# Kernel optimization log

Hardware: AMD Instinct MI355X
Metric: run time of the kernel (lower is better)

## Reference

```python
import jax, jax.numpy as jnp
import numpy as np

N, E, H, IN = 4096, 65536, 256, 16
N_BLOCKS, N_SUB = 3, 2
IE = 2 * H + 2  # edge-mlp input: h[row] ++ h[col] ++ edge_attr(2)
NORM_FACTOR = 100.0


def setup_inputs() -> dict:
    key = jax.random.key(0)
    ks = jax.random.split(key, 24)
    G = N_BLOCKS * N_SUB  # 6 GCLs total

    def p(k, shape, fan_in, gain=1.0):
        return gain * jax.random.normal(k, shape, jnp.float32) / np.sqrt(fan_in)

    return {
        "h": jax.random.normal(ks[0], (N, IN), jnp.float32),
        "x": jax.random.normal(ks[1], (N, 3), jnp.float32),
        "edge_index": jax.random.randint(ks[2], (2, E), 0, N),
        # embedding in/out
        "emb_w": p(ks[3], (IN, H), IN), "emb_b": jnp.zeros((H,), jnp.float32),
        "out_w": p(ks[4], (H, IN), H), "out_b": jnp.zeros((IN,), jnp.float32),
        # GCL edge MLP (stacked over the 6 GCLs)
        "edge_w1": p(ks[5], (G, IE, H), IE), "edge_b1": jnp.zeros((G, H), jnp.float32),
        "edge_w2": p(ks[6], (G, H, H), H), "edge_b2": jnp.zeros((G, H), jnp.float32),
        # GCL node MLP
        "node_w1": p(ks[7], (G, 2 * H, H), 2 * H), "node_b1": jnp.zeros((G, H), jnp.float32),
        "node_w2": p(ks[8], (G, H, H), H), "node_b2": jnp.zeros((G, H), jnp.float32),
        # EquivariantUpdate coord MLP (stacked over 3 blocks); last layer xavier gain=0.001, no bias
        "coord_w1": p(ks[9], (N_BLOCKS, IE, H), IE), "coord_b1": jnp.zeros((N_BLOCKS, H), jnp.float32),
        "coord_w2": p(ks[10], (N_BLOCKS, H, H), H), "coord_b2": jnp.zeros((N_BLOCKS, H), jnp.float32),
        "coord_w3": p(ks[11], (N_BLOCKS, H, 1), H, gain=0.001),
    }


def reference(h, x, edge_index, emb_w, emb_b, out_w, out_b,
              edge_w1, edge_b1, edge_w2, edge_b2,
              node_w1, node_b1, node_w2, node_b2,
              coord_w1, coord_b1, coord_w2, coord_b2, coord_w3):
    row, col = edge_index[0], edge_index[1]
    n_nodes = h.shape[0]

    def seg_sum(data):  # unsorted_segment_sum with 'sum' aggregation / normalization_factor
        return jax.ops.segment_sum(data, row, num_segments=n_nodes) / NORM_FACTOR

    def coord2diff(xc):  # norm_constant = 1
        d = xc[row] - xc[col]                      # [E,3]
        radial = jnp.sum(d * d, axis=1, keepdims=True)  # [E,1]
        cd = d / (jnp.sqrt(radial + 1e-8) + 1.0)
        return radial, cd

    dist0, _ = coord2diff(x)          # EGNN-level distances (from initial coords)
    h = h @ emb_w + emb_b             # node embedding

    gi = 0
    for b in range(N_BLOCKS):
        radial, coord_diff = coord2diff(x)
        ea = jnp.concatenate([radial, dist0], axis=1)   # [E,2] edge_attr
        for _ in range(N_SUB):  # GCL sublayers
            m = jnp.concatenate([h[row], h[col], ea], axis=1)           # [E, 2H+2]
            m = jax.nn.silu(m @ edge_w1[gi] + edge_b1[gi])
            m = jax.nn.silu(m @ edge_w2[gi] + edge_b2[gi])              # [E, H]
            agg = seg_sum(m)                                            # [N, H]
            u = jnp.concatenate([h, agg], axis=1)                       # [N, 2H]
            u = jax.nn.silu(u @ node_w1[gi] + node_b1[gi])
            h = h + u @ node_w2[gi] + node_b2[gi]                       # residual node update
            gi += 1
        # EquivariantUpdate (tanh=False)
        t = jnp.concatenate([h[row], h[col], ea], axis=1)
        t = jax.nn.silu(t @ coord_w1[b] + coord_b1[b])
        t = jax.nn.silu(t @ coord_w2[b] + coord_b2[b])
        trans = coord_diff * (t @ coord_w3[b])                          # [E,3]
        x = x + seg_sum(trans)

    h = h @ out_w + out_b
    return h, x
```

## Files before the change

kernel.cpp:

```cpp
#include <hip/hip_runtime.h>
#include <hip/hip_bf16.h>
#include <cstdint>
#include <cstddef>

#define NN 4096
#define NE 65536
#define HD 256

typedef __attribute__((ext_vector_type(4))) float f32x4;
typedef __attribute__((ext_vector_type(8))) __bf16 bf16x8;

static __device__ __forceinline__ float silu_f(float v) {
  return v / (1.f + __expf(-v));
}

struct TJob { const float* src; __bf16* dst; int K; int N; };
struct TJobs { TJob j[39]; };

__global__ __launch_bounds__(256) void k_transpose(TJobs jobs) {
  TJob jb = jobs.j[blockIdx.z];
  int k0 = blockIdx.x << 5, n0 = blockIdx.y << 5;
  if (k0 >= jb.K || n0 >= jb.N) return;
  __shared__ float t[32][33];
  int tx = threadIdx.x & 31, ty = threadIdx.x >> 5;
#pragma unroll
  for (int r = ty; r < 32; r += 8)
    t[r][tx] = jb.src[(size_t)(k0 + r) * jb.N + n0 + tx];
  __syncthreads();
#pragma unroll
  for (int r = ty; r < 32; r += 8)
    jb.dst[(size_t)(n0 + r) * jb.K + k0 + tx] = (__bf16)t[tx][r];
}

__global__ __launch_bounds__(256) void k_hist(const int* __restrict__ ei, int* __restrict__ cnt) {
  int e = blockIdx.x * 256 + threadIdx.x;
  atomicAdd(&cnt[ei[e]], 1);
}

__global__ __launch_bounds__(1024) void k_scan(const int* __restrict__ cnt, int* __restrict__ offs,
                                               int* __restrict__ cursor) {
  __shared__ int tmp[1024];
  int tid = threadIdx.x;
  int v[4]; int s = 0;
#pragma unroll
  for (int i = 0; i < 4; i++) { v[i] = cnt[tid * 4 + i]; s += v[i]; }
  tmp[tid] = s;
  __syncthreads();
  for (int o = 1; o < 1024; o <<= 1) {
    int t = (tid >= o) ? tmp[tid - o] : 0;
    __syncthreads();
    tmp[tid] += t;
    __syncthreads();
  }
  int base = (tid > 0) ? tmp[tid - 1] : 0;
#pragma unroll
  for (int i = 0; i < 4; i++) {
    offs[tid * 4 + i] = base; cursor[tid * 4 + i] = base; base += v[i];
  }
  if (tid == 1023) offs[4096] = base;
}

__global__ __launch_bounds__(256) void k_scatter(const int* __restrict__ ei, int* __restrict__ cursor,
                                                 int* __restrict__ elist) {
  int e = blockIdx.x * 256 + threadIdx.x;
  int pos = atomicAdd(&cursor[ei[e]], 1);
  elist[pos] = e;
}

__global__ __launch_bounds__(256) void k_csrinit(const int* __restrict__ elist, const int* __restrict__ ei,
                                                 const float* __restrict__ x, int* __restrict__ rowp,
                                                 int* __restrict__ colp, float* __restrict__ d0p) {
  int i = blockIdx.x * 256 + threadIdx.x;
  int e = elist[i];
  int r = ei[e], c = ei[NE + e];
  rowp[i] = r; colp[i] = c;
  float dx = x[r * 3 + 0] - x[c * 3 + 0];
  float dy = x[r * 3 + 1] - x[c * 3 + 1];
  float dz = x[r * 3 + 2] - x[c * 3 + 2];
  d0p[i] = dx * dx + dy * dy + dz * dz;
}

__global__ __launch_bounds__(256) void k_geo(const int* __restrict__ rowp, const int* __restrict__ colp,
                                             const float* __restrict__ x, float* __restrict__ radp,
                                             float* __restrict__ cdp) {
  int i = blockIdx.x * 256 + threadIdx.x;
  int r = rowp[i], c = colp[i];
  float dx = x[r * 3 + 0] - x[c * 3 + 0];
  float dy = x[r * 3 + 1] - x[c * 3 + 1];
  float dz = x[r * 3 + 2] - x[c * 3 + 2];
  float rad = dx * dx + dy * dy + dz * dz;
  radp[i] = rad;
  float inv = 1.f / (sqrtf(rad + 1e-8f) + 1.f);
  cdp[i * 3 + 0] = dx * inv; cdp[i * 3 + 1] = dy * inv; cdp[i * 3 + 2] = dz * inv;
}

__global__ __launch_bounds__(256) void k_copyx(const float* __restrict__ x, float* __restrict__ xc) {
  int i = blockIdx.x * 256 + threadIdx.x;
  if (i < NN * 3) xc[i] = x[i];
}

__global__ __launch_bounds__(256) void k_embed(const float* __restrict__ h0, const float* __restrict__ W,
                                               const float* __restrict__ b, float* __restrict__ hf,
                                               __bf16* __restrict__ h16) {
  int n = blockIdx.x, c = threadIdx.x;
  float s = b[c];
#pragma unroll
  for (int i = 0; i < 16; i++) s += h0[n * 16 + i] * W[i * 256 + c];
  hf[(size_t)n * HD + c] = s;
  h16[(size_t)n * HD + c] = (__bf16)s;
}

__global__ __launch_bounds__(256) void k_segsum(const __bf16* __restrict__ m2p, const int* __restrict__ offs,
                                                const __bf16* __restrict__ h16, __bf16* __restrict__ ncat) {
  __shared__ float sd[8][256];
  int n = blockIdx.x, t = threadIdx.x;
  int g = t >> 5, l = t & 31;
  int c0 = l << 3;
  float a[8] = {};
  int ib = offs[n], ie = offs[n + 1];
  for (int i = ib + g; i < ie; i += 8) {
    bf16x8 v = *(const bf16x8*)(m2p + (size_t)i * 256 + c0);
#pragma unroll
    for (int j = 0; j < 8; j++) a[j] += (float)v[j];
  }
#pragma unroll
  for (int j = 0; j < 8; j++) sd[g][c0 + j] = a[j];
  __syncthreads();
  float s = 0.f;
#pragma unroll
  for (int j = 0; j < 8; j++) s += sd[j][t];
  ncat[(size_t)n * 512 + t] = h16[(size_t)n * HD + t];
  ncat[(size_t)n * 512 + 256 + t] = (__bf16)(s * 0.01f);
}

__global__ __launch_bounds__(256) void k_xupd(const float* __restrict__ transp, const int* __restrict__ offs,
                                              float* __restrict__ xc) {
  int n = blockIdx.x * 256 + threadIdx.x;
  if (n >= NN) return;
  float a0 = 0.f, a1 = 0.f, a2 = 0.f;
  int i1 = offs[n + 1];
  for (int i = offs[n]; i < i1; i++) {
    a0 += transp[i * 3 + 0]; a1 += transp[i * 3 + 1]; a2 += transp[i * 3 + 2];
  }
  xc[n * 3 + 0] += a0 * 0.01f;
  xc[n * 3 + 1] += a1 * 0.01f;
  xc[n * 3 + 2] += a2 * 0.01f;
}

__global__ __launch_bounds__(256) void k_outh(const float* __restrict__ hf, const float* __restrict__ W,
                                              const float* __restrict__ b, float* __restrict__ out) {
  int t = blockIdx.x * 256 + threadIdx.x;
  int n = t >> 4, j = t & 15;
  float s = b[j];
  for (int c = 0; c < 256; c++) s += hf[(size_t)n * HD + c] * W[c * 16 + j];
  out[n * 16 + j] = s;
}

__global__ __launch_bounds__(256) void k_outx(const float* __restrict__ xc, float* __restrict__ out) {
  int i = blockIdx.x * 256 + threadIdx.x;
  if (i < NN * 3) out[i] = xc[i];
}

template <int EPI>
__global__ __launch_bounds__(512, 2) void k_edgeblk(
    const __bf16* __restrict__ PQ, const int* __restrict__ rowp, const int* __restrict__ colp,
    const float* __restrict__ radp, const float* __restrict__ d0p,
    const float* __restrict__ w1r, const float* __restrict__ w1d, const float* __restrict__ b1,
    const __bf16* __restrict__ Bt, const float* __restrict__ b2,
    __bf16* __restrict__ m2p,
    const float* __restrict__ w3, const float* __restrict__ cdp, float* __restrict__ transp) {
  constexpr int BM = 128, BK = 32;
  __shared__ __bf16 As[2][BM * BK];
  __shared__ __bf16 Bs[2][256 * BK];
  __shared__ float reds[BM][2];
  const int tid = threadIdx.x;
  const int lane = tid & 63;
  const int wave = tid >> 6;
  const int wm = wave >> 1, wn = wave & 1;
  const int m0 = blockIdx.x * BM;

  const int ar = tid >> 2, aq = tid & 3;
  const int er = rowp[m0 + ar], ec = colp[m0 + ar];
  const float rad = radp[m0 + ar], dd0 = d0p[m0 + ar];
  const int aswz = (ar >> 1) & 3;
  const int br = tid >> 1, bg0 = (tid & 1) * 2;
  const int bswz = (br >> 1) & 3;

  f32x4 acc[2][8] = {};

  {
    bf16x8 pv = *(const bf16x8*)(PQ + (size_t)er * 512 + aq * 8);
    bf16x8 qv = *(const bf16x8*)(PQ + (size_t)ec * 512 + 256 + aq * 8);
    float4 wra = *(const float4*)(w1r + aq * 8), wrb = *(const float4*)(w1r + aq * 8 + 4);
    float4 wda = *(const float4*)(w1d + aq * 8), wdb = *(const float4*)(w1d + aq * 8 + 4);
    float4 b1a = *(const float4*)(b1 + aq * 8), b1b = *(const float4*)(b1 + aq * 8 + 4);
    bf16x8 o;
    const float* wr4 = &wra.x; const float* wd4 = &wda.x; const float* bb4 = &b1a.x;
#pragma unroll
    for (int j = 0; j < 4; j++)
      o[j] = (__bf16)silu_f((float)pv[j] + (float)qv[j] + rad * wr4[j] + dd0 * wd4[j] + bb4[j]);
    const float* wr4b = &wrb.x; const float* wd4b = &wdb.x; const float* bb4b = &b1b.x;
#pragma unroll
    for (int j = 0; j < 4; j++)
      o[4 + j] = (__bf16)silu_f((float)pv[4 + j] + (float)qv[4 + j] + rad * wr4b[j] + dd0 * wd4b[j] + bb4b[j]);
    *(bf16x8*)&As[0][ar * BK + ((aq ^ aswz) << 3)] = o;
    bf16x8 v0 = *(const bf16x8*)(Bt + (size_t)br * 256 + bg0 * 8);
    bf16x8 v1 = *(const bf16x8*)(Bt + (size_t)br * 256 + bg0 * 8 + 8);
    *(bf16x8*)&Bs[0][br * BK + ((bg0 ^ bswz) << 3)] = v0;
    *(bf16x8*)&Bs[0][br * BK + (((bg0 + 1) ^ bswz) << 3)] = v1;
  }
  __syncthreads();

  int buf = 0;
  for (int t = 0; t < 8; ++t) {
    const int ktn = (t + 1) * BK;
    const bool has = (t < 7);
    bf16x8 pv, qv, v0, v1;
    float4 wra, wrb, wda, wdb, b1a, b1b;
    if (has) {
      pv = *(const bf16x8*)(PQ + (size_t)er * 512 + ktn + aq * 8);
      qv = *(const bf16x8*)(PQ + (size_t)ec * 512 + 256 + ktn + aq * 8);
      wra = *(const float4*)(w1r + ktn + aq * 8); wrb = *(const float4*)(w1r + ktn + aq * 8 + 4);
      wda = *(const float4*)(w1d + ktn + aq * 8); wdb = *(const float4*)(w1d + ktn + aq * 8 + 4);
      b1a = *(const float4*)(b1 + ktn + aq * 8);  b1b = *(const float4*)(b1 + ktn + aq * 8 + 4);
      v0 = *(const bf16x8*)(Bt + (size_t)br * 256 + ktn + bg0 * 8);
      v1 = *(const bf16x8*)(Bt + (size_t)br * 256 + ktn + bg0 * 8 + 8);
    }
    const int kg = lane >> 4;
    bf16x8 af[2];
#pragma unroll
    for (int fm = 0; fm < 2; fm++) {
      int r = wm * 32 + fm * 16 + (lane & 15);
      af[fm] = *(const bf16x8*)&As[buf][r * BK + ((kg ^ ((r >> 1) & 3)) << 3)];
    }
#pragma unroll
    for (int fn = 0; fn < 8; fn++) {
      int r = wn * 128 + fn * 16 + (lane & 15);
      bf16x8 bf = *(const bf16x8*)&Bs[buf][r * BK + ((kg ^ ((r >> 1) & 3)) << 3)];
#pragma unroll
      for (int fm = 0; fm < 2; fm++)
        acc[fm][fn] = __builtin_amdgcn_mfma_f32_16x16x32_bf16(af[fm], bf, acc[fm][fn], 0, 0, 0);
    }
    if (has) {
      bf16x8 o;
      const float* wr4 = &wra.x; const float* wd4 = &wda.x; const float* bb4 = &b1a.x;
#pragma unroll
      for (int j = 0; j < 4; j++)
        o[j] = (__bf16)silu_f((float)pv[j] + (float)qv[j] + rad * wr4[j] + dd0 * wd4[j] + bb4[j]);
      const float* wr4b = &wrb.x; const float* wd4b = &wdb.x; const float* bb4b = &b1b.x;
#pragma unroll
      for (int j = 0; j < 4; j++)
        o[4 + j] = (__bf16)silu_f((float)pv[4 + j] + (float)qv[4 + j] + rad * wr4b[j] + dd0 * wd4b[j] + bb4b[j]);
      *(bf16x8*)&As[buf ^ 1][ar * BK + ((aq ^ aswz) << 3)] = o;
      *(bf16x8*)&Bs[buf ^ 1][br * BK + ((bg0 ^ bswz) << 3)] = v0;
      *(bf16x8*)&Bs[buf ^ 1][br * BK + (((bg0 + 1) ^ bswz) << 3)] = v1;
    }
    __syncthreads();
    buf ^= 1;
  }

  if (EPI == 0) {
#pragma unroll
    for (int fn = 0; fn < 8; fn++) {
      int col = wn * 128 + fn * 16 + (lane & 15);
      float bv = b2[col];
#pragma unroll
      for (int fm = 0; fm < 2; fm++) {
#pragma unroll
        for (int j = 0; j < 4; j++) {
          int row = m0 + wm * 32 + fm * 16 + ((lane >> 4) << 2) + j;
          m2p[(size_t)row * 256 + col] = (__bf16)silu_f(acc[fm][fn][j] + bv);
        }
      }
    }
  } else {
    float s[2][4] = {};
#pragma unroll
    for (int fn = 0; fn < 8; fn++) {
      int col = wn * 128 + fn * 16 + (lane & 15);
      float bv = b2[col], wv = w3[col];
#pragma unroll
      for (int fm = 0; fm < 2; fm++)
#pragma unroll
        for (int j = 0; j < 4; j++)
          s[fm][j] += silu_f(acc[fm][fn][j] + bv) * wv;
    }
#pragma unroll
    for (int off = 1; off < 16; off <<= 1)
#pragma unroll
      for (int fm = 0; fm < 2; fm++)
#pragma unroll
        for (int j = 0; j < 4; j++)
          s[fm][j] += __shfl_xor(s[fm][j], off, 64);
    if ((lane & 15) == 0) {
#pragma unroll
      for (int fm = 0; fm < 2; fm++)
#pragma unroll
        for (int j = 0; j < 4; j++)
          reds[wm * 32 + fm * 16 + ((lane >> 4) << 2) + j][wn] = s[fm][j];
    }
    __syncthreads();
    if (tid < BM) {
      float sv = reds[tid][0] + reds[tid][1];
      size_t i = (size_t)m0 + tid;
      transp[i * 3 + 0] = cdp[i * 3 + 0] * sv;
      transp[i * 3 + 1] = cdp[i * 3 + 1] * sv;
      transp[i * 3 + 2] = cdp[i * 3 + 2] * sv;
    }
  }
}

template <int EPI>
__global__ __launch_bounds__(256) void k_gemm64(const __bf16* __restrict__ A, const __bf16* __restrict__ Bt,
                                                const float* __restrict__ bias, __bf16* __restrict__ outb,
                                                float* __restrict__ outf, int M, int N, int K) {
  constexpr int BM = 64, BN = 64, BK = 64;
  __shared__ __bf16 As[2][BM * BK];
  __shared__ __bf16 Bs[2][BN * BK];
  const int tid = threadIdx.x;
  const int lane = tid & 63;
  const int wave = tid >> 6;
  const int wm = wave >> 1, wn = wave & 1;
  const size_t m0 = (size_t)blockIdx.x * BM;
  const size_t n0 = (size_t)blockIdx.y * BN;
  const int r0 = tid >> 3, g0 = tid & 7;
  const int gs0 = (g0 ^ (r0 & 7)) << 3;

  f32x4 acc[2][2] = {};
  const int NT = K >> 6;

  {
    uint4 a0 = *(const uint4*)(A + (m0 + r0) * K + g0 * 8);
    uint4 a1 = *(const uint4*)(A + (m0 + r0 + 32) * K + g0 * 8);
    uint4 b0 = *(const uint4*)(Bt + (n0 + r0) * K + g0 * 8);
    uint4 b1 = *(const uint4*)(Bt + (n0 + r0 + 32) * K + g0 * 8);
    *(uint4*)&As[0][r0 * BK + gs0] = a0;
    *(uint4*)&As[0][(r0 + 32) * BK + gs0] = a1;
    *(uint4*)&Bs[0][r0 * BK + gs0] = b0;
    *(uint4*)&Bs[0][(r0 + 32) * BK + gs0] = b1;
  }
  __syncthreads();

  int buf = 0;
  for (int t = 0; t < NT; ++t) {
    const bool has = (t + 1 < NT);
    uint4 a0, a1, b0, b1;
    if (has) {
      int kt = (t + 1) << 6;
      a0 = *(const uint4*)(A + (m0 + r0) * K + kt + g0 * 8);
      a1 = *(const uint4*)(A + (m0 + r0 + 32) * K + kt + g0 * 8);
      b0 = *(const uint4*)(Bt + (n0 + r0) * K + kt + g0 * 8);
      b1 = *(const uint4*)(Bt + (n0 + r0 + 32) * K + kt + g0 * 8);
    }
#pragma unroll
    for (int ks = 0; ks < BK; ks += 32) {
      const int kg = (ks >> 3) + (lane >> 4);
      bf16x8 af[2], bfv[2];
#pragma unroll
      for (int fm = 0; fm < 2; fm++) {
        int r = wm * 32 + fm * 16 + (lane & 15);
        af[fm] = *(const bf16x8*)&As[buf][r * BK + ((kg ^ (r & 7)) << 3)];
      }
#pragma unroll
      for (int fn = 0; fn < 2; fn++) {
        int r = wn * 32 + fn * 16 + (lane & 15);
        bfv[fn] = *(const bf16x8*)&Bs[buf][r * BK + ((kg ^ (r & 7)) << 3)];
      }
#pragma unroll
      for (int fm = 0; fm < 2; fm++)
#pragma unroll
        for (int fn = 0; fn < 2; fn++)
          acc[fm][fn] = __builtin_amdgcn_mfma_f32_16x16x32_bf16(af[fm], bfv[fn], acc[fm][fn], 0, 0, 0);
    }
    if (has) {
      *(uint4*)&As[buf ^ 1][r0 * BK + gs0] = a0;
      *(uint4*)&As[buf ^ 1][(r0 + 32) * BK + gs0] = a1;
      *(uint4*)&Bs[buf ^ 1][r0 * BK + gs0] = b0;
      *(uint4*)&Bs[buf ^ 1][(r0 + 32) * BK + gs0] = b1;
    }
    __syncthreads();
    buf ^= 1;
  }

#pragma unroll
  for (int fm = 0; fm < 2; fm++) {
#pragma unroll
    for (int fn = 0; fn < 2; fn++) {
      const size_t col = n0 + wn * 32 + fn * 16 + (lane & 15);
      float bv = (EPI == 4) ? 0.f : bias[col];
#pragma unroll
      for (int j = 0; j < 4; j++) {
        size_t row = m0 + wm * 32 + fm * 16 + ((lane >> 4) << 2) + j;
        size_t idx = row * (size_t)N + col;
        float v = acc[fm][fn][j] + bv;
        if (EPI == 1) {
          outb[idx] = (__bf16)silu_f(v);
        } else if (EPI == 2) {
          float nh = outf[idx] + v;
          outf[idx] = nh;
          outb[idx] = (__bf16)nh;
        } else {
          outb[idx] = (__bf16)v;
        }
      }
    }
  }
}

extern "C" void kernel_launch(void* const* d_in, const int* in_sizes, int n_in,
                              void* d_out, int out_size, void* d_ws, size_t ws_size,
                              hipStream_t stream) {
  const float* h_in    = (const float*)d_in[0];
  const float* x_in    = (const float*)d_in[1];
  const int*   ei      = (const int*)d_in[2];
  const float* emb_w   = (const float*)d_in[3];
  const float* emb_b   = (const float*)d_in[4];
  const float* out_w   = (const float*)d_in[5];
  const float* out_b   = (const float*)d_in[6];
  const float* edge_w1 = (const float*)d_in[7];
  const float* edge_b1 = (const float*)d_in[8];
  const float* edge_w2 = (const float*)d_in[9];
  const float* edge_b2 = (const float*)d_in[10];
  const float* node_w1 = (const float*)d_in[11];
  const float* node_b1 = (const float*)d_in[12];
  const float* node_w2 = (const float*)d_in[13];
  const float* node_b2 = (const float*)d_in[14];
  const float* coord_w1 = (const float*)d_in[15];
  const float* coord_b1 = (const float*)d_in[16];
  const float* coord_w2 = (const float*)d_in[17];
  const float* coord_b2 = (const float*)d_in[18];
  const float* coord_w3 = (const float*)d_in[19];

  char* p = (char*)d_ws;
  auto alloc = [&](size_t bytes) -> void* {
    void* r = (void*)p;
    p += (bytes + 255) & ~(size_t)255;
    return r;
  };
  __bf16* e1T  = (__bf16*)alloc((size_t)6 * 512 * 256 * 2);
  __bf16* e2T  = (__bf16*)alloc((size_t)6 * 256 * 256 * 2);
  __bf16* n1T  = (__bf16*)alloc((size_t)6 * 256 * 512 * 2);
  __bf16* n2T  = (__bf16*)alloc((size_t)6 * 256 * 256 * 2);
  __bf16* c1T  = (__bf16*)alloc((size_t)3 * 512 * 256 * 2);
  __bf16* c2T  = (__bf16*)alloc((size_t)3 * 256 * 256 * 2);
  __bf16* h16  = (__bf16*)alloc((size_t)NN * HD * 2);
  __bf16* PQ16 = (__bf16*)alloc((size_t)NN * 512 * 2);
  __bf16* m2p  = (__bf16*)alloc((size_t)NE * HD * 2);
  __bf16* ncat = (__bf16*)alloc((size_t)NN * 512 * 2);
  __bf16* u    = (__bf16*)alloc((size_t)NN * HD * 2);
  float* hf    = (float*)alloc((size_t)NN * HD * 4);
  float* xc    = (float*)alloc((size_t)NN * 3 * 4);
  float* d0p   = (float*)alloc((size_t)NE * 4);
  float* radp  = (float*)alloc((size_t)NE * 4);
  float* cdp   = (float*)alloc((size_t)NE * 3 * 4);
  float* transp = (float*)alloc((size_t)NE * 3 * 4);
  int* cnt     = (int*)alloc((size_t)NN * 4);
  int* offs    = (int*)alloc((size_t)(NN + 1) * 4);
  int* cursor  = (int*)alloc((size_t)NN * 4);
  int* elist   = (int*)alloc((size_t)NE * 4);
  int* rowp    = (int*)alloc((size_t)NE * 4);
  int* colp    = (int*)alloc((size_t)NE * 4);

  TJobs jobs;
  int nj = 0;
  for (int gi = 0; gi < 6; gi++) {
    jobs.j[nj++] = { edge_w1 + (size_t)gi * 514 * 256,             e1T + (size_t)gi * 512 * 256,             256, 256 };
    jobs.j[nj++] = { edge_w1 + (size_t)gi * 514 * 256 + 256 * 256, e1T + (size_t)gi * 512 * 256 + 256 * 256, 256, 256 };
    jobs.j[nj++] = { edge_w2 + (size_t)gi * 256 * 256,             e2T + (size_t)gi * 256 * 256,             256, 256 };
    jobs.j[nj++] = { node_w1 + (size_t)gi * 512 * 256,             n1T + (size_t)gi * 256 * 512,             512, 256 };
    jobs.j[nj++] = { node_w2 + (size_t)gi * 256 * 256,             n2T + (size_t)gi * 256 * 256,             256, 256 };
  }
  for (int b = 0; b < 3; b++) {
    jobs.j[nj++] = { coord_w1 + (size_t)b * 514 * 256,             c1T + (size_t)b * 512 * 256,              256, 256 };
    jobs.j[nj++] = { coord_w1 + (size_t)b * 514 * 256 + 256 * 256, c1T + (size_t)b * 512 * 256 + 256 * 256,  256, 256 };
    jobs.j[nj++] = { coord_w2 + (size_t)b * 256 * 256,             c2T + (size_t)b * 256 * 256,              256, 256 };
  }

  hipMemsetAsync(cnt, 0, (size_t)NN * 4, stream);
  k_transpose<<<dim3(16, 8, 39), 256, 0, stream>>>(jobs);
  k_hist<<<NE / 256, 256, 0, stream>>>(ei, cnt);
  k_scan<<<1, 1024, 0, stream>>>(cnt, offs, cursor);
  k_scatter<<<NE / 256, 256, 0, stream>>>(ei, cursor, elist);
  k_csrinit<<<NE / 256, 256, 0, stream>>>(elist, ei, x_in, rowp, colp, d0p);
  k_copyx<<<(NN * 3 + 255) / 256, 256, 0, stream>>>(x_in, xc);
  k_embed<<<NN, 256, 0, stream>>>(h_in, emb_w, emb_b, hf, h16);

  int gi = 0;
  for (int b = 0; b < 3; b++) {
    k_geo<<<NE / 256, 256, 0, stream>>>(rowp, colp, xc, radp, cdp);
    for (int s = 0; s < 2; s++, gi++) {
      const float* w1 = edge_w1 + (size_t)gi * 514 * 256;
      k_gemm64<4><<<dim3(64, 8), 256, 0, stream>>>(
          h16, e1T + (size_t)gi * 512 * 256, nullptr, PQ16, nullptr, NN, 512, 256);
      k_edgeblk<0><<<NE / 128, 512, 0, stream>>>(
          PQ16, rowp, colp, radp, d0p, w1 + 512 * 256, w1 + 513 * 256, edge_b1 + gi * 256,
          e2T + (size_t)gi * 256 * 256, edge_b2 + gi * 256, m2p, nullptr, nullptr, nullptr);
      k_segsum<<<NN, 256, 0, stream>>>(m2p, offs, h16, ncat);
      k_gemm64<1><<<dim3(64, 4), 256, 0, stream>>>(
          ncat, n1T + (size_t)gi * 256 * 512, node_b1 + gi * 256, u, nullptr, NN, 256, 512);
      k_gemm64<2><<<dim3(64, 4), 256, 0, stream>>>(
          u, n2T + (size_t)gi * 256 * 256, node_b2 + gi * 256, h16, hf, NN, 256, 256);
    }
    const float* w1c = coord_w1 + (size_t)b * 514 * 256;
    k_gemm64<4><<<dim3(64, 8), 256, 0, stream>>>(
        h16, c1T + (size_t)b * 512 * 256, nullptr, PQ16, nullptr, NN, 512, 256);
    k_edgeblk<1><<<NE / 128, 512, 0, stream>>>(
        PQ16, rowp, colp, radp, d0p, w1c + 512 * 256, w1c + 513 * 256, coord_b1 + b * 256,
        c2T + (size_t)b * 256 * 256, coord_b2 + b * 256, nullptr,
        coord_w3 + (size_t)b * 256, cdp, transp);
    k_xupd<<<NN / 256, 256, 0, stream>>>(transp, offs, xc);
  }
  k_outh<<<NN * 16 / 256, 256, 0, stream>>>(hf, out_w, out_b, (float*)d_out);
  k_outx<<<(NN * 3 + 255) / 256, 256, 0, stream>>>(xc, (float*)d_out + (size_t)NN * 16);
}
```

Measured before the change: 571.3 us.

## Stage full activated A tile in LDS and re-tile edge MLP waves 2x4

```diff
diff --git a/kernel.cpp b/kernel.cpp
--- a/kernel.cpp
+++ b/kernel.cpp
@@ -162,125 +162,125 @@
 }
 
 template <int EPI>
-__global__ __launch_bounds__(512, 2) void k_edgeblk(
+__global__ __launch_bounds__(512, 4) void k_edgeblk(
     const __bf16* __restrict__ PQ, const int* __restrict__ rowp, const int* __restrict__ colp,
     const float* __restrict__ radp, const float* __restrict__ d0p,
     const float* __restrict__ w1r, const float* __restrict__ w1d, const float* __restrict__ b1,
     const __bf16* __restrict__ Bt, const float* __restrict__ b2,
     __bf16* __restrict__ m2p,
     const float* __restrict__ w3, const float* __restrict__ cdp, float* __restrict__ transp) {
-  constexpr int BM = 128, BK = 32;
-  __shared__ __bf16 As[2][BM * BK];
-  __shared__ __bf16 Bs[2][256 * BK];
-  __shared__ float reds[BM][2];
+  __shared__ alignas(16) char smem[81920];
+  __bf16* As = (__bf16*)smem;
+  __bf16* Bs = (__bf16*)(smem + 65536);
+  float (*reds)[4] = (float(*)[4])smem;
+
   const int tid = threadIdx.x;
   const int lane = tid & 63;
   const int wave = tid >> 6;
-  const int wm = wave >> 1, wn = wave & 1;
-  const int m0 = blockIdx.x * BM;
-
-  const int ar = tid >> 2, aq = tid & 3;
+  const int wm = wave >> 2, wn = wave & 3;
+  const int m0 = blockIdx.x * 128;
+
+  const int bn = tid >> 1;
+  const int bg = (tid & 1) * 2;
+  const int bswz0 = (bg ^ ((bn >> 1) & 3)) << 3;
+  const int bswz1 = ((bg + 1) ^ ((bn >> 1) & 3)) << 3;
+
+  const int ar = tid >> 2;
+  const int aq = tid & 3;
   const int er = rowp[m0 + ar], ec = colp[m0 + ar];
   const float rad = radp[m0 + ar], dd0 = d0p[m0 + ar];
-  const int aswz = (ar >> 1) & 3;
-  const int br = tid >> 1, bg0 = (tid & 1) * 2;
-  const int bswz = (br >> 1) & 3;
-
-  f32x4 acc[2][8] = {};
-
-  {
-    bf16x8 pv = *(const bf16x8*)(PQ + (size_t)er * 512 + aq * 8);
-    bf16x8 qv = *(const bf16x8*)(PQ + (size_t)ec * 512 + 256 + aq * 8);
-    float4 wra = *(const float4*)(w1r + aq * 8), wrb = *(const float4*)(w1r + aq * 8 + 4);
-    float4 wda = *(const float4*)(w1d + aq * 8), wdb = *(const float4*)(w1d + aq * 8 + 4);
-    float4 b1a = *(const float4*)(b1 + aq * 8), b1b = *(const float4*)(b1 + aq * 8 + 4);
+
+  uint4 br0a = *(const uint4*)(Bt + (size_t)bn * 256 + bg * 8);
+  uint4 br0b = *(const uint4*)(Bt + (size_t)bn * 256 + bg * 8 + 8);
+  uint4 br1a = *(const uint4*)(Bt + (size_t)bn * 256 + 32 + bg * 8);
+  uint4 br1b = *(const uint4*)(Bt + (size_t)bn * 256 + 32 + bg * 8 + 8);
+  uint4 breg[2][2];
+  breg[0][0] = br0a; breg[0][1] = br0b;
+  breg[1][0] = br1a; breg[1][1] = br1b;
+
+#pragma unroll
+  for (int i = 0; i < 8; i++) {
+    int g = aq + 4 * i;
+    int k = g * 8;
+    bf16x8 pv = *(const bf16x8*)(PQ + (size_t)er * 512 + k);
+    bf16x8 qv = *(const bf16x8*)(PQ + (size_t)ec * 512 + 256 + k);
+    float4 wr0 = *(const float4*)(w1r + k),     wr1 = *(const float4*)(w1r + k + 4);
+    float4 wd0 = *(const float4*)(w1d + k),     wd1 = *(const float4*)(w1d + k + 4);
+    float4 bb0 = *(const float4*)(b1 + k),      bb1 = *(const float4*)(b1 + k + 4);
     bf16x8 o;
-    const float* wr4 = &wra.x; const float* wd4 = &wda.x; const float* bb4 = &b1a.x;
+    const float* wrp0 = &wr0.x; const float* wdp0 = &wd0.x; const float* bbp0 = &bb0.x;
 #pragma unroll
     for (int j = 0; j < 4; j++)
-      o[j] = (__bf16)silu_f((float)pv[j] + (float)qv[j] + rad * wr4[j] + dd0 * wd4[j] + bb4[j]);
-    const float* wr4b = &wrb.x; const float* wd4b = &wdb.x; const float* bb4b = &b1b.x;
+      o[j] = (__bf16)silu_f((float)pv[j] + (float)qv[j] + rad * wrp0[j] + dd0 * wdp0[j] + bbp0[j]);
+    const float* wrp1 = &wr1.x; const float* wdp1 = &wd1.x; const float* bbp1 = &bb1.x;
 #pragma unroll
     for (int j = 0; j < 4; j++)
-      o[4 + j] = (__bf16)silu_f((float)pv[4 + j] + (float)qv[4 + j] + rad * wr4b[j] + dd0 * wd4b[j] + bb4b[j]);
-    *(bf16x8*)&As[0][ar * BK + ((aq ^ aswz) << 3)] = o;
-    bf16x8 v0 = *(const bf16x8*)(Bt + (size_t)br * 256 + bg0 * 8);
-    bf16x8 v1 = *(const bf16x8*)(Bt + (size_t)br * 256 + bg0 * 8 + 8);
-    *(bf16x8*)&Bs[0][br * BK + ((bg0 ^ bswz) << 3)] = v0;
-    *(bf16x8*)&Bs[0][br * BK + (((bg0 + 1) ^ bswz) << 3)] = v1;
-  }
+      o[4 + j] = (__bf16)silu_f((float)pv[4 + j] + (float)qv[4 + j] + rad * wrp1[j] + dd0 * wdp1[j] + bbp1[j]);
+    *(bf16x8*)&As[ar * 256 + ((g ^ (ar & 7)) << 3)] = o;
+  }
+
+  *(uint4*)&Bs[bn * 32 + bswz0] = breg[0][0];
+  *(uint4*)&Bs[bn * 32 + bswz1] = breg[0][1];
   __syncthreads();
 
-  int buf = 0;
-  for (int t = 0; t < 8; ++t) {
-    const int ktn = (t + 1) * BK;
-    const bool has = (t < 7);
-    bf16x8 pv, qv, v0, v1;
-    float4 wra, wrb, wda, wdb, b1a, b1b;
-    if (has) {
-      pv = *(const bf16x8*)(PQ + (size_t)er * 512 + ktn + aq * 8);
-      qv = *(const bf16x8*)(PQ + (size_t)ec * 512 + 256 + ktn + aq * 8);
-      wra = *(const float4*)(w1r + ktn + aq * 8); wrb = *(const float4*)(w1r + ktn + aq * 8 + 4);
-      wda = *(const float4*)(w1d + ktn + aq * 8); wdb = *(const float4*)(w1d + ktn + aq * 8 + 4);
-      b1a = *(const float4*)(b1 + ktn + aq * 8);  b1b = *(const float4*)(b1 + ktn + aq * 8 + 4);
-      v0 = *(const bf16x8*)(Bt + (size_t)br * 256 + ktn + bg0 * 8);
-      v1 = *(const bf16x8*)(Bt + (size_t)br * 256 + ktn + bg0 * 8 + 8);
-    }
-    const int kg = lane >> 4;
-    bf16x8 af[2];
-#pragma unroll
-    for (int fm = 0; fm < 2; fm++) {
-      int r = wm * 32 + fm * 16 + (lane & 15);
-      af[fm] = *(const bf16x8*)&As[buf][r * BK + ((kg ^ ((r >> 1) & 3)) << 3)];
-    }
-#pragma unroll
-    for (int fn = 0; fn < 8; fn++) {
-      int r = wn * 128 + fn * 16 + (lane & 15);
-      bf16x8 bf = *(const bf16x8*)&Bs[buf][r * BK + ((kg ^ ((r >> 1) & 3)) << 3)];
-#pragma unroll
-      for (int fm = 0; fm < 2; fm++)
-        acc[fm][fn] = __builtin_amdgcn_mfma_f32_16x16x32_bf16(af[fm], bf, acc[fm][fn], 0, 0, 0);
-    }
-    if (has) {
-      bf16x8 o;
-      const float* wr4 = &wra.x; const float* wd4 = &wda.x; const float* bb4 = &b1a.x;
-#pragma unroll
-      for (int j = 0; j < 4; j++)
-        o[j] = (__bf16)silu_f((float)pv[j] + (float)qv[j] + rad * wr4[j] + dd0 * wd4[j] + bb4[j]);
-      const float* wr4b = &wrb.x; const float* wd4b = &wdb.x; const float* bb4b = &b1b.x;
-#pragma unroll
-      for (int j = 0; j < 4; j++)
-        o[4 + j] = (__bf16)silu_f((float)pv[4 + j] + (float)qv[4 + j] + rad * wr4b[j] + dd0 * wd4b[j] + bb4b[j]);
-      *(bf16x8*)&As[buf ^ 1][ar * BK + ((aq ^ aswz) << 3)] = o;
-      *(bf16x8*)&Bs[buf ^ 1][br * BK + ((bg0 ^ bswz) << 3)] = v0;
-      *(bf16x8*)&Bs[buf ^ 1][br * BK + (((bg0 + 1) ^ bswz) << 3)] = v1;
+  f32x4 acc[4][4] = {};
+  const int kg = lane >> 4;
+  const int l15 = lane & 15;
+
+#pragma unroll
+  for (int t = 0; t < 8; t++) {
+    if (t + 2 < 8) {
+      breg[t & 1][0] = *(const uint4*)(Bt + (size_t)bn * 256 + (t + 2) * 32 + bg * 8);
+      breg[t & 1][1] = *(const uint4*)(Bt + (size_t)bn * 256 + (t + 2) * 32 + bg * 8 + 8);
+    }
+    bf16x8 bf[4];
+#pragma unroll
+    for (int fn = 0; fn < 4; fn++) {
+      int n = wn * 64 + fn * 16 + l15;
+      bf[fn] = *(const bf16x8*)&Bs[n * 32 + ((kg ^ ((n >> 1) & 3)) << 3)];
+    }
+#pragma unroll
+    for (int fm = 0; fm < 4; fm++) {
+      int r = wm * 64 + fm * 16 + l15;
+      int G = t * 4 + kg;
+      bf16x8 af = *(const bf16x8*)&As[r * 256 + ((G ^ (r & 7)) << 3)];
+#pragma unroll
+      for (int fn = 0; fn < 4; fn++)
+        acc[fm][fn] = __builtin_amdgcn_mfma_f32_16x16x32_bf16(af, bf[fn], acc[fm][fn], 0, 0, 0);
     }
     __syncthreads();
-    buf ^= 1;
+    if (t < 7) {
+      *(uint4*)&Bs[bn * 32 + bswz0] = breg[(t + 1) & 1][0];
+      *(uint4*)&Bs[bn * 32 + bswz1] = breg[(t + 1) & 1][1];
+      __syncthreads();
+    }
   }
 
   if (EPI == 0) {
 #pragma unroll
-    for (int fn = 0; fn < 8; fn++) {
-      int col = wn * 128 + fn * 16 + (lane & 15);
-      float bv = b2[col];
-#pragma unroll
-      for (int fm = 0; fm < 2; fm++) {
-#pragma unroll
-        for (int j = 0; j < 4; j++) {
-          int row = m0 + wm * 32 + fm * 16 + ((lane >> 4) << 2) + j;
-          m2p[(size_t)row * 256 + col] = (__bf16)silu_f(acc[fm][fn][j] + bv);
+    for (int fm = 0; fm < 4; fm++) {
+#pragma unroll
+      for (int j = 0; j < 4; j++) {
+        size_t row = m0 + wm * 64 + fm * 16 + ((lane >> 4) << 2) + j;
+#pragma unroll
+        for (int fn = 0; fn < 4; fn++) {
+          int col = wn * 64 + fn * 16 + l15;
+          m2p[row * 256 + col] = (__bf16)silu_f(acc[fm][fn][j] + b2[col]);
         }
       }
     }
   } else {
-    float s[2][4] = {};
-#pragma unroll
-    for (int fn = 0; fn < 8; fn++) {
-      int col = wn * 128 + fn * 16 + (lane & 15);
+    float s[4][4];
+#pragma unroll
+    for (int fm = 0; fm < 4; fm++)
+#pragma unroll
+      for (int j = 0; j < 4; j++) s[fm][j] = 0.f;
+#pragma unroll
+    for (int fn = 0; fn < 4; fn++) {
+      int col = wn * 64 + fn * 16 + l15;
       float bv = b2[col], wv = w3[col];
 #pragma unroll
-      for (int fm = 0; fm < 2; fm++)
+      for (int fm = 0; fm < 4; fm++)
 #pragma unroll
         for (int j = 0; j < 4; j++)
           s[fm][j] += silu_f(acc[fm][fn][j] + bv) * wv;
@@ -288,20 +288,20 @@
 #pragma unroll
     for (int off = 1; off < 16; off <<= 1)
 #pragma unroll
-      for (int fm = 0; fm < 2; fm++)
+      for (int fm = 0; fm < 4; fm++)
 #pragma unroll
         for (int j = 0; j < 4; j++)
           s[fm][j] += __shfl_xor(s[fm][j], off, 64);
-    if ((lane & 15) == 0) {
-#pragma unroll
-      for (int fm = 0; fm < 2; fm++)
+    if (l15 == 0) {
+#pragma unroll
+      for (int fm = 0; fm < 4; fm++)
 #pragma unroll
         for (int j = 0; j < 4; j++)
-          reds[wm * 32 + fm * 16 + ((lane >> 4) << 2) + j][wn] = s[fm][j];
+          reds[wm * 64 + fm * 16 + ((lane >> 4) << 2) + j][wn] = s[fm][j];
     }
     __syncthreads();
-    if (tid < BM) {
-      float sv = reds[tid][0] + reds[tid][1];
+    if (tid < 128) {
+      float sv = reds[tid][0] + reds[tid][1] + reds[tid][2] + reds[tid][3];
       size_t i = (size_t)m0 + tid;
       transp[i * 3 + 0] = cdp[i * 3 + 0] * sv;
       transp[i * 3 + 1] = cdp[i * 3 + 1] * sv;
```

Result: faster. 516.3 us (-9.6%).
